# Performance work log

Measured on AMD Instinct MI355X. Metric: run time of the kernel, lower is better.

## Reference

```python
import jax, jax.numpy as jnp
import numpy as np

E = 1024
H = 16
D = E // H  # head_dim = 64
FF = 4 * E
EPS = 1e-5


def layernorm(x, g, b):
    mu = jnp.mean(x, axis=-1, keepdims=True)
    var = jnp.var(x, axis=-1, keepdims=True)
    return (x - mu) * jax.lax.rsqrt(var + EPS) * g + b


def setup_inputs() -> dict:
    key = jax.random.key(0)
    ks = jax.random.split(key, 12)
    s = 1.0 / np.sqrt(E)
    sf = 1.0 / np.sqrt(FF)
    return {
        "x": jax.random.normal(ks[0], (2, 2048, E), dtype=jnp.float32),
        "wq": jax.random.uniform(ks[1], (E, E), jnp.float32, -s, s),
        "wk": jax.random.uniform(ks[2], (E, E), jnp.float32, -s, s),
        "wv": jax.random.uniform(ks[3], (E, E), jnp.float32, -s, s),
        "wo": jax.random.uniform(ks[4], (E, E), jnp.float32, -s, s),
        "bo": jax.random.uniform(ks[5], (E,), jnp.float32, -s, s),
        "g1": jnp.ones((E,), jnp.float32),
        "b1": jnp.zeros((E,), jnp.float32),
        "w1": jax.random.uniform(ks[6], (FF, E), jnp.float32, -s, s),
        "bf1": jax.random.uniform(ks[7], (FF,), jnp.float32, -s, s),
        "w2": jax.random.uniform(ks[8], (E, FF), jnp.float32, -sf, sf),
        "bf2": jax.random.uniform(ks[9], (E,), jnp.float32, -sf, sf),
        "g2": jnp.ones((E,), jnp.float32),
        "b2": jnp.zeros((E,), jnp.float32),
    }


def reference(x, wq, wk, wv, wo, bo, g1, b1, w1, bf1, w2, bf2, g2, b2):
    B, L, _ = x.shape
    # projections (torch Linear: x @ W.T)
    q = (x @ wq.T).reshape(B, L, H, D).transpose(0, 2, 1, 3)  # (B,H,L,D)
    k = (x @ wk.T).reshape(B, L, H, D).transpose(0, 2, 1, 3)
    v = (x @ wv.T).reshape(B, L, H, D).transpose(0, 2, 1, 3)
    scores = jnp.einsum('bhqd,bhkd->bhqk', q, k) / np.sqrt(D)
    attn = jax.nn.softmax(scores, axis=-1)
    ctx = jnp.einsum('bhqk,bhkd->bhqd', attn, v)
    ctx = ctx.transpose(0, 2, 1, 3).reshape(B, L, E)
    attn_out = ctx @ wo.T + bo
    h = layernorm(x + attn_out, g1, b1)
    ff = jax.nn.gelu(h @ w1.T + bf1, approximate=False) @ w2.T + bf2
    return layernorm(h + ff, g2, b2)
```

## Files before the change

### kernel.cpp

```cpp
#include <hip/hip_runtime.h>
#include <hip/hip_bf16.h>
#include <stdint.h>

typedef __bf16 bf16x8 __attribute__((ext_vector_type(8)));
typedef float  f32x4  __attribute__((ext_vector_type(4)));
typedef unsigned short u16;
typedef u16 u16x8 __attribute__((ext_vector_type(8)));

__device__ __forceinline__ u16 f2b(float f) {
  uint32_t u = __builtin_bit_cast(uint32_t, f);
  u += 0x7fffu + ((u >> 16) & 1u);
  return (u16)(u >> 16);
}

__device__ __forceinline__ f32x4 mfma16(bf16x8 a, bf16x8 b, f32x4 c) {
  return __builtin_amdgcn_mfma_f32_16x16x32_bf16(a, b, c, 0, 0, 0);
}

__device__ __forceinline__ void gload_lds16(const void* g, void* l) {
  __builtin_amdgcn_global_load_lds(
      (const __attribute__((address_space(1))) void*)g,
      (__attribute__((address_space(3))) void*)l, 16, 0, 0);
}

#define BARRIER() asm volatile("s_barrier" ::: "memory")
#define LGKM0()   asm volatile("s_waitcnt lgkmcnt(0)" ::: "memory")

__global__ void f2b_all(const float* __restrict__ x,  const float* __restrict__ wq,
                        const float* __restrict__ wk, const float* __restrict__ wv,
                        const float* __restrict__ wo, const float* __restrict__ w1,
                        const float* __restrict__ w2,
                        u16* __restrict__ xb, u16* __restrict__ wqkvb,
                        u16* __restrict__ wob, u16* __restrict__ w1b,
                        u16* __restrict__ w2b) {
  const int i = blockIdx.x * blockDim.x + threadIdx.x;
  const float* src; u16* dst; int off;
  if (i < 524288)        { src = x;  dst = xb;              off = i; }
  else if (i < 655360)   { src = wq; dst = wqkvb;           off = i - 524288; }
  else if (i < 786432)   { src = wk; dst = wqkvb + 1048576; off = i - 655360; }
  else if (i < 917504)   { src = wv; dst = wqkvb + 2097152; off = i - 786432; }
  else if (i < 1048576)  { src = wo; dst = wob;             off = i - 917504; }
  else if (i < 1572864)  { src = w1; dst = w1b;             off = i - 1048576; }
  else                   { src = w2; dst = w2b;             off = i - 1572864; }
  const float4* p = (const float4*)src + (size_t)off * 2;
  float4 a = p[0], b = p[1];
  u16x8 r;
  r[0] = f2b(a.x); r[1] = f2b(a.y); r[2] = f2b(a.z); r[3] = f2b(a.w);
  r[4] = f2b(b.x); r[5] = f2b(b.y); r[6] = f2b(b.z); r[7] = f2b(b.w);
  *((u16x8*)dst + off) = r;
}

template<int MODE>
__global__ __launch_bounds__(512, 2) void gemm256(
    const u16* __restrict__ A, const u16* __restrict__ W,
    const float* __restrict__ bias,
    void* __restrict__ o0, void* __restrict__ o1,
    void* __restrict__ o2, void* __restrict__ o3,
    int Nsz, int Kstride, int Klen, int ntiles)
{
  __shared__ u16 As[2][2][8192];
  __shared__ u16 Bs[2][2][8192];

  const int nbn = Nsz >> 8;
  int bid = blockIdx.x;
  bid = (bid & 7) * ((int)gridDim.x >> 3) + (bid >> 3);
  const int tile = (MODE == 1) ? (bid % ntiles) : bid;
  const int sid  = (MODE == 1) ? (bid / ntiles) : 0;
  const int koff = sid * Klen;
  const int bm = tile / nbn;
  const int bn = tile % nbn;
  const int tid = threadIdx.x;
  const int w = tid >> 6, l = tid & 63;
  const int lh = l >> 4, ll = l & 15;
  const int wm = w >> 2, wn = w & 3;

  f32x4 acc[8][4] = {};

  const u16* Ag = A + (size_t)(bm * 256) * Kstride + koff;
  const u16* Wg = W + (size_t)(bn * 256) * Kstride + koff;

  const int r0 = tid >> 3, s0 = tid & 7;
  const int sg = s0 ^ (r0 & 7);
  const int NT = Klen >> 6;

  auto stage = [&](int t, int H) {
    const int b = t & 1;
    const size_t ce = (size_t)t * 64 + sg * 8;
    const u16* G = (H < 2) ? Ag : Wg;
    u16* D = (H < 2) ? &As[b][H & 1][0] : &Bs[b][H & 1][0];
    const int gr = (H & 1) * 128;
    gload_lds16(G + (size_t)(gr + r0) * Kstride + ce, D + tid * 8);
    gload_lds16(G + (size_t)(gr + r0 + 64) * Kstride + ce, D + (512 + tid) * 8);
  };

  auto dsA = [&](int p, int mi, int kk) -> bf16x8 {
    const int r = mi * 16 + ll;
    return *(const bf16x8*)(&As[p][wm][0] + r * 64 + (((kk * 4 + lh) ^ (ll & 7)) * 8));
  };
  auto dsB = [&](int p, int ni, int kk) -> bf16x8 {
    const int r = (wn & 1) * 64 + ni * 16 + ll;
    return *(const bf16x8*)(&Bs[p][wn >> 1][0] + r * 64 + (((kk * 4 + lh) ^ (ll & 7)) * 8));
  };

  stage(0, 0); stage(0, 1); stage(0, 2); stage(0, 3);
  asm volatile("s_waitcnt vmcnt(0)" ::: "memory");
  BARRIER();

  bf16x8 bq[4], aq[4];
  for (int t = 0; t < NT; ++t) {
    const int p = t & 1;
    const bool st = (t + 1 < NT);

#pragma unroll
    for (int ni = 0; ni < 4; ++ni) bq[ni] = dsB(p, ni, 0);
#pragma unroll
    for (int m2 = 0; m2 < 4; ++m2) aq[m2] = dsA(p, m2, 0);
    if (st) stage(t + 1, 0);
    BARRIER(); LGKM0();
    __builtin_amdgcn_s_setprio(1);
#pragma unroll
    for (int m2 = 0; m2 < 4; ++m2)
#pragma unroll
      for (int ni = 0; ni < 4; ++ni)
        acc[m2][ni] = mfma16(aq[m2], bq[ni], acc[m2][ni]);
    __builtin_amdgcn_s_setprio(0);
    BARRIER();

#pragma unroll
    for (int m2 = 0; m2 < 4; ++m2) aq[m2] = dsA(p, 4 + m2, 0);
    if (st) stage(t + 1, 1);
    BARRIER(); LGKM0();
    __builtin_amdgcn_s_setprio(1);
#pragma unroll
    for (int m2 = 0; m2 < 4; ++m2)
#pragma unroll
      for (int ni = 0; ni < 4; ++ni)
        acc[4 + m2][ni] = mfma16(aq[m2], bq[ni], acc[4 + m2][ni]);
    __builtin_amdgcn_s_setprio(0);
    BARRIER();

#pragma unroll
    for (int ni = 0; ni < 4; ++ni) bq[ni] = dsB(p, ni, 1);
#pragma unroll
    for (int m2 = 0; m2 < 4; ++m2) aq[m2] = dsA(p, m2, 1);
    if (st) stage(t + 1, 2);
    BARRIER(); LGKM0();
    __builtin_amdgcn_s_setprio(1);
#pragma unroll
    for (int m2 = 0; m2 < 4; ++m2)
#pragma unroll
      for (int ni = 0; ni < 4; ++ni)
        acc[m2][ni] = mfma16(aq[m2], bq[ni], acc[m2][ni]);
    __builtin_amdgcn_s_setprio(0);
    BARRIER();

#pragma unroll
    for (int m2 = 0; m2 < 4; ++m2) aq[m2] = dsA(p, 4 + m2, 1);
    if (st) stage(t + 1, 3);
    BARRIER(); LGKM0();
    __builtin_amdgcn_s_setprio(1);
#pragma unroll
    for (int m2 = 0; m2 < 4; ++m2)
#pragma unroll
      for (int ni = 0; ni < 4; ++ni)
        acc[4 + m2][ni] = mfma16(aq[m2], bq[ni], acc[4 + m2][ni]);
    __builtin_amdgcn_s_setprio(0);
    if (st) asm volatile("s_waitcnt vmcnt(0)" ::: "memory");
    BARRIER();
  }

#pragma unroll
  for (int mi = 0; mi < 8; ++mi) {
#pragma unroll
    for (int ni = 0; ni < 4; ++ni) {
      const int col = bn * 256 + wn * 64 + ni * 16 + ll;
#pragma unroll
      for (int i = 0; i < 4; ++i) {
        const int row = bm * 256 + wm * 128 + mi * 16 + lh * 4 + i;
        float v = acc[mi][ni][i];
        if (MODE == 1) {
          float* dst = (sid == 0) ? (float*)o0 : (sid == 1) ? (float*)o1
                     : (sid == 2) ? (float*)o2 : (float*)o3;
          dst[(size_t)row * Nsz + col] = v;
        } else if (MODE == 2) {
          float xx = v + bias[col];
          float gl = 0.5f * xx * (1.0f + erff(xx * 0.70710678118654752f));
          ((u16*)o0)[(size_t)row * Nsz + col] = f2b(gl);
        } else {
          const int which = col >> 10;
          const int e = col & 1023;
          const int hh = e >> 6, dd = e & 63;
          const int bb = row >> 11, nl = row & 2047;
          if (which == 0) {
            ((u16*)o0)[((size_t)(bb * 16 + hh) * 2048 + nl) * 64 + dd] = f2b(v * 0.18033688f);
          } else if (which == 1) {
            ((u16*)o1)[((size_t)(bb * 16 + hh) * 2048 + nl) * 64 + dd] = f2b(v);
          } else {
            ((u16*)o2)[((size_t)(bb * 16 + hh) * 64 + dd) * 2048 + nl] = f2b(v);
          }
        }
      }
    }
  }
}

__global__ __launch_bounds__(256, 4) void attn_fwd(
    const u16* __restrict__ Q, const u16* __restrict__ K,
    const u16* __restrict__ Vt, u16* __restrict__ ctx)
{
  __shared__ u16 Ks[2][64 * 64];
  __shared__ u16 Vs[2][64 * 64];
  __shared__ u16 Ps[4][16 * 64];

  const int bh = blockIdx.x & 31;
  const int qt = blockIdx.x >> 5;
  const int tid = threadIdx.x;
  const int w = tid >> 6, l = tid & 63;
  const int lh = l >> 4, ll = l & 15;
  const int q0 = qt * 64 + w * 16;

  bf16x8 qf[2];
  {
    const u16* Qg = Q + ((size_t)bh * 2048 + q0 + ll) * 64;
#pragma unroll
    for (int kk = 0; kk < 2; ++kk)
      qf[kk] = *(const bf16x8*)(Qg + kk * 32 + lh * 8);
  }

  bf16x8 ones;
  {
    const u16 o = 0x3F80;
#pragma unroll
    for (int i = 0; i < 8; ++i) ones[i] = __builtin_bit_cast(__bf16, o);
  }

  f32x4 cacc[4] = {};
  f32x4 lacc = {};
  float m_l = -1e30f;
  u16* ps = Ps[w];

  const int f0 = tid, f1 = 256 + tid;
  const int r0 = f0 >> 3, s0 = f0 & 7, g0 = (s0 ^ (r0 & 7)) * 8;
  const int r1 = f1 >> 3, s1 = f1 & 7, g1 = (s1 ^ (r1 & 7)) * 8;

  {
    gload_lds16(K + ((size_t)bh * 2048 + r0) * 64 + g0, Ks[0] + f0 * 8);
    gload_lds16(Vt + ((size_t)bh * 64 + r0) * 2048 + g0, Vs[0] + f0 * 8);
    gload_lds16(K + ((size_t)bh * 2048 + r1) * 64 + g1, Ks[0] + f1 * 8);
    gload_lds16(Vt + ((size_t)bh * 64 + r1) * 2048 + g1, Vs[0] + f1 * 8);
  }
  __syncthreads();

  for (int kt = 0; kt < 32; ++kt) {
    const int b = kt & 1;
    if (kt < 31) {
      const int kn = (kt + 1) * 64;
      gload_lds16(K + ((size_t)bh * 2048 + kn + r0) * 64 + g0, Ks[b ^ 1] + f0 * 8);
      gload_lds16(Vt + ((size_t)bh * 64 + r0) * 2048 + kn + g0, Vs[b ^ 1] + f0 * 8);
      gload_lds16(K + ((size_t)bh * 2048 + kn + r1) * 64 + g1, Ks[b ^ 1] + f1 * 8);
      gload_lds16(Vt + ((size_t)bh * 64 + r1) * 2048 + kn + g1, Vs[b ^ 1] + f1 * 8);
    }

    f32x4 st[4];
    __builtin_amdgcn_s_setprio(1);
#pragma unroll
    for (int jb = 0; jb < 4; ++jb) {
      f32x4 a = {};
#pragma unroll
      for (int kk = 0; kk < 2; ++kk) {
        const int r = jb * 16 + ll;
        bf16x8 kf = *(const bf16x8*)(Ks[b] + r * 64 + (((kk * 4 + lh) ^ (r & 7)) * 8));
        a = mfma16(kf, qf[kk], a);
      }
      st[jb] = a;
    }
    __builtin_amdgcn_s_setprio(0);

    float mx = fmaxf(fmaxf(fmaxf(st[0][0], st[0][1]), fmaxf(st[0][2], st[0][3])),
                     fmaxf(fmaxf(st[1][0], st[1][1]), fmaxf(st[1][2], st[1][3])));
    mx = fmaxf(mx, fmaxf(fmaxf(fmaxf(st[2][0], st[2][1]), fmaxf(st[2][2], st[2][3])),
                         fmaxf(fmaxf(st[3][0], st[3][1]), fmaxf(st[3][2], st[3][3]))));
    mx = fmaxf(mx, __shfl_xor(mx, 16));
    mx = fmaxf(mx, __shfl_xor(mx, 32));

    if (!__all(mx - m_l <= 8.0f)) {
      const float mn = fmaxf(m_l, mx);
      const float al = __builtin_amdgcn_exp2f(m_l - mn);
      m_l = mn;
      float alq[4];
#pragma unroll
      for (int i = 0; i < 4; ++i) alq[i] = __shfl(al, lh * 4 + i);
#pragma unroll
      for (int db = 0; db < 4; ++db)
#pragma unroll
        for (int i = 0; i < 4; ++i) cacc[db][i] *= alq[i];
#pragma unroll
      for (int i = 0; i < 4; ++i) lacc[i] *= alq[i];
    }

#pragma unroll
    for (int jb = 0; jb < 4; ++jb) {
      const float p0 = __builtin_amdgcn_exp2f(st[jb][0] - m_l);
      const float p1 = __builtin_amdgcn_exp2f(st[jb][1] - m_l);
      const float p2 = __builtin_amdgcn_exp2f(st[jb][2] - m_l);
      const float p3 = __builtin_amdgcn_exp2f(st[jb][3] - m_l);
      uint2 pk;
      asm("v_cvt_pk_bf16_f32 %0, %1, %2" : "=v"(pk.x) : "v"(p0), "v"(p1));
      asm("v_cvt_pk_bf16_f32 %0, %1, %2" : "=v"(pk.y) : "v"(p2), "v"(p3));
      *(uint2*)(ps + ll * 64 + (((jb * 2 + (lh >> 1)) ^ (ll & 7)) * 8) + (lh & 1) * 4) = pk;
    }

    asm volatile("s_waitcnt lgkmcnt(0)" ::: "memory");
    __builtin_amdgcn_sched_barrier(0);

    __builtin_amdgcn_s_setprio(1);
#pragma unroll
    for (int kk = 0; kk < 2; ++kk) {
      bf16x8 pf = *(const bf16x8*)(ps + ll * 64 + (((kk * 4 + lh) ^ (ll & 7)) * 8));
      lacc = mfma16(pf, ones, lacc);
#pragma unroll
      for (int db = 0; db < 4; ++db) {
        const int vr = db * 16 + ll;
        bf16x8 vf = *(const bf16x8*)(Vs[b] + vr * 64 + (((kk * 4 + lh) ^ (vr & 7)) * 8));
        cacc[db] = mfma16(pf, vf, cacc[db]);
      }
    }
    __builtin_amdgcn_s_setprio(0);
    __syncthreads();
  }

  const int bb = bh >> 4, hh = bh & 15;
#pragma unroll
  for (int db = 0; db < 4; ++db)
#pragma unroll
    for (int i = 0; i < 4; ++i) {
      const float v = cacc[db][i] / lacc[i];
      const size_t orow = (size_t)bb * 2048 + q0 + lh * 4 + i;
      const size_t ocol = (size_t)hh * 64 + db * 16 + ll;
      ctx[orow * 1024 + ocol] = f2b(v);
    }
}

__global__ __launch_bounds__(256) void ln_fused(
    const float* __restrict__ a,  const float* __restrict__ b0,
    const float* __restrict__ b1, const float* __restrict__ b2,
    const float* __restrict__ b3, const float* __restrict__ bias,
    const float* __restrict__ g,  const float* __restrict__ be,
    float* __restrict__ ho, u16* __restrict__ hb)
{
  const int row = blockIdx.x;
  const int t = threadIdx.x;
  const size_t base = (size_t)row * 1024 + t * 4;
  float4 xa = *(const float4*)(a + base);
  float4 xb = *(const float4*)(b0 + base);
  float v0 = xa.x + xb.x, v1 = xa.y + xb.y, v2 = xa.z + xb.z, v3 = xa.w + xb.w;
  if (b1) {
    float4 xc = *(const float4*)(b1 + base);
    v0 += xc.x; v1 += xc.y; v2 += xc.z; v3 += xc.w;
  }
  if (b2) {
    float4 xc = *(const float4*)(b2 + base);
    v0 += xc.x; v1 += xc.y; v2 += xc.z; v3 += xc.w;
  }
  if (b3) {
    float4 xc = *(const float4*)(b3 + base);
    v0 += xc.x; v1 += xc.y; v2 += xc.z; v3 += xc.w;
  }
  if (bias) {
    float4 xd = *(const float4*)(bias + t * 4);
    v0 += xd.x; v1 += xd.y; v2 += xd.z; v3 += xd.w;
  }
  float s = v0 + v1 + v2 + v3;
  float ss = v0 * v0 + v1 * v1 + v2 * v2 + v3 * v3;
#pragma unroll
  for (int d = 1; d < 64; d <<= 1) {
    s += __shfl_xor(s, d);
    ss += __shfl_xor(ss, d);
  }
  __shared__ float red[8];
  const int w = t >> 6, lid = t & 63;
  if (lid == 0) { red[w] = s; red[4 + w] = ss; }
  __syncthreads();
  s = red[0] + red[1] + red[2] + red[3];
  ss = red[4] + red[5] + red[6] + red[7];
  const float mean = s * (1.0f / 1024.0f);
  const float var = ss * (1.0f / 1024.0f) - mean * mean;
  const float rstd = rsqrtf(var + 1e-5f);
  const float vv[4] = {v0, v1, v2, v3};
#pragma unroll
  for (int i = 0; i < 4; ++i) {
    const int col = t * 4 + i;
    const float hv = (vv[i] - mean) * rstd * g[col] + be[col];
    if (ho) ho[base + i] = hv;
    if (hb) hb[base + i] = f2b(hv);
  }
}

extern "C" void kernel_launch(void* const* d_in, const int* in_sizes, int n_in,
                              void* d_out, int out_size, void* d_ws, size_t ws_size,
                              hipStream_t stream) {
  const float* x   = (const float*)d_in[0];
  const float* wq  = (const float*)d_in[1];
  const float* wk  = (const float*)d_in[2];
  const float* wv  = (const float*)d_in[3];
  const float* wo  = (const float*)d_in[4];
  const float* bo  = (const float*)d_in[5];
  const float* g1  = (const float*)d_in[6];
  const float* b1  = (const float*)d_in[7];
  const float* w1  = (const float*)d_in[8];
  const float* bf1 = (const float*)d_in[9];
  const float* w2  = (const float*)d_in[10];
  const float* bf2 = (const float*)d_in[11];
  const float* g2  = (const float*)d_in[12];
  const float* b2  = (const float*)d_in[13];

  char* ws = (char*)d_ws;
  const size_t MB = 1u << 20;
  u16* xb    = (u16*)(ws + 0);
  u16* wqkv  = (u16*)(ws + 8 * MB);
  u16* wob   = (u16*)(ws + 14 * MB);
  u16* w1b   = (u16*)(ws + 16 * MB);
  u16* w2b   = (u16*)(ws + 24 * MB);
  u16* qb    = (u16*)(ws + 32 * MB);
  u16* kb    = (u16*)(ws + 40 * MB);
  u16* vtb   = (u16*)(ws + 48 * MB);
  u16* ctxb  = (u16*)(ws + 56 * MB);
  float* pA   = (float*)(ws + 64 * MB);
  float* hbuf = (float*)(ws + 80 * MB);
  u16* hbb   = (u16*)(ws + 96 * MB);
  float* wo_p1 = (float*)(ws + 32 * MB);
  u16* ff1   = (u16*)(ws + 32 * MB);
  float* f2_p1 = (float*)(ws + 0);
  float* f2_p2 = (float*)(ws + 48 * MB);
  float* f2_p3 = (float*)d_out;

  f2b_all<<<8192, 256, 0, stream>>>(x, wq, wk, wv, wo, w1, w2, xb, wqkv, wob, w1b, w2b);

  gemm256<0><<<192, 512, 0, stream>>>(xb, wqkv, nullptr, qb, kb, vtb, nullptr,
                                      3072, 1024, 1024, 0);
  attn_fwd<<<1024, 256, 0, stream>>>(qb, kb, vtb, ctxb);
  gemm256<1><<<128, 512, 0, stream>>>(ctxb, wob, nullptr, pA, wo_p1, nullptr, nullptr,
                                      1024, 1024, 512, 64);
  ln_fused<<<4096, 256, 0, stream>>>(x, pA, wo_p1, nullptr, nullptr, bo, g1, b1, hbuf, hbb);
  gemm256<2><<<256, 512, 0, stream>>>(hbb, w1b, bf1, ff1, nullptr, nullptr, nullptr,
                                      4096, 1024, 1024, 0);
  gemm256<1><<<256, 512, 0, stream>>>(ff1, w2b, nullptr, pA, f2_p1, f2_p2, f2_p3,
                                      1024, 4096, 1024, 64);
  ln_fused<<<4096, 256, 0, stream>>>(hbuf, pA, f2_p1, f2_p2, f2_p3, bf2, g2, b2,
                                     (float*)d_out, nullptr);
}
```

Measured before the change: 294.0 us.

## Restage GEMM LDS by K-halves with partial vmcnt waits and 2-way FF2 split-K

```diff
diff --git a/kernel.cpp b/kernel.cpp
--- a/kernel.cpp
+++ b/kernel.cpp
@@ -58,8 +58,8 @@
     void* __restrict__ o2, void* __restrict__ o3,
     int Nsz, int Kstride, int Klen, int ntiles)
 {
-  __shared__ u16 As[2][2][8192];
-  __shared__ u16 Bs[2][2][8192];
+  __shared__ u16 As[2][2][256 * 32];
+  __shared__ u16 Bs[2][2][256 * 32];
 
   const int nbn = Nsz >> 8;
   int bid = blockIdx.x;
@@ -79,34 +79,33 @@
   const u16* Ag = A + (size_t)(bm * 256) * Kstride + koff;
   const u16* Wg = W + (size_t)(bn * 256) * Kstride + koff;
 
-  const int r0 = tid >> 3, s0 = tid & 7;
-  const int sg = s0 ^ (r0 & 7);
+  const int r0 = tid >> 2;
+  const int sg = (tid & 3) ^ (r0 & 3);
   const int NT = Klen >> 6;
 
   auto stage = [&](int t, int H) {
-    const int b = t & 1;
-    const size_t ce = (size_t)t * 64 + sg * 8;
-    const u16* G = (H < 2) ? Ag : Wg;
-    u16* D = (H < 2) ? &As[b][H & 1][0] : &Bs[b][H & 1][0];
-    const int gr = (H & 1) * 128;
-    gload_lds16(G + (size_t)(gr + r0) * Kstride + ce, D + tid * 8);
-    gload_lds16(G + (size_t)(gr + r0 + 64) * Kstride + ce, D + (512 + tid) * 8);
+    const int b = t & 1, kk = H >> 1;
+    const u16* G = (H & 1) ? Wg : Ag;
+    u16* D = (H & 1) ? &Bs[b][kk][0] : &As[b][kk][0];
+    const size_t ce = (size_t)t * 64 + kk * 32 + sg * 8;
+    gload_lds16(G + (size_t)r0 * Kstride + ce,         D + tid * 8);
+    gload_lds16(G + (size_t)(r0 + 128) * Kstride + ce, D + (512 + tid) * 8);
   };
 
   auto dsA = [&](int p, int mi, int kk) -> bf16x8 {
-    const int r = mi * 16 + ll;
-    return *(const bf16x8*)(&As[p][wm][0] + r * 64 + (((kk * 4 + lh) ^ (ll & 7)) * 8));
+    const int r = wm * 128 + mi * 16 + ll;
+    return *(const bf16x8*)(&As[p][kk][0] + r * 32 + ((lh ^ (ll & 3)) * 8));
   };
   auto dsB = [&](int p, int ni, int kk) -> bf16x8 {
-    const int r = (wn & 1) * 64 + ni * 16 + ll;
-    return *(const bf16x8*)(&Bs[p][wn >> 1][0] + r * 64 + (((kk * 4 + lh) ^ (ll & 7)) * 8));
+    const int r = wn * 64 + ni * 16 + ll;
+    return *(const bf16x8*)(&Bs[p][kk][0] + r * 32 + ((lh ^ (ll & 3)) * 8));
   };
 
   stage(0, 0); stage(0, 1); stage(0, 2); stage(0, 3);
   asm volatile("s_waitcnt vmcnt(0)" ::: "memory");
   BARRIER();
 
-  bf16x8 bq[4], aq[4];
+  bf16x8 aq[4], bq[4];
   for (int t = 0; t < NT; ++t) {
     const int p = t & 1;
     const bool st = (t + 1 < NT);
@@ -116,7 +115,7 @@
 #pragma unroll
     for (int m2 = 0; m2 < 4; ++m2) aq[m2] = dsA(p, m2, 0);
     if (st) stage(t + 1, 0);
-    BARRIER(); LGKM0();
+    BARRIER(); LGKM0(); __builtin_amdgcn_sched_barrier(0);
     __builtin_amdgcn_s_setprio(1);
 #pragma unroll
     for (int m2 = 0; m2 < 4; ++m2)
@@ -129,7 +128,7 @@
 #pragma unroll
     for (int m2 = 0; m2 < 4; ++m2) aq[m2] = dsA(p, 4 + m2, 0);
     if (st) stage(t + 1, 1);
-    BARRIER(); LGKM0();
+    BARRIER(); LGKM0(); __builtin_amdgcn_sched_barrier(0);
     __builtin_amdgcn_s_setprio(1);
 #pragma unroll
     for (int m2 = 0; m2 < 4; ++m2)
@@ -137,6 +136,8 @@
       for (int ni = 0; ni < 4; ++ni)
         acc[4 + m2][ni] = mfma16(aq[m2], bq[ni], acc[4 + m2][ni]);
     __builtin_amdgcn_s_setprio(0);
+    if (st) asm volatile("s_waitcnt vmcnt(4)" ::: "memory");
+    else    asm volatile("s_waitcnt vmcnt(0)" ::: "memory");
     BARRIER();
 
 #pragma unroll
@@ -144,7 +145,7 @@
 #pragma unroll
     for (int m2 = 0; m2 < 4; ++m2) aq[m2] = dsA(p, m2, 1);
     if (st) stage(t + 1, 2);
-    BARRIER(); LGKM0();
+    BARRIER(); LGKM0(); __builtin_amdgcn_sched_barrier(0);
     __builtin_amdgcn_s_setprio(1);
 #pragma unroll
     for (int m2 = 0; m2 < 4; ++m2)
@@ -157,7 +158,7 @@
 #pragma unroll
     for (int m2 = 0; m2 < 4; ++m2) aq[m2] = dsA(p, 4 + m2, 1);
     if (st) stage(t + 1, 3);
-    BARRIER(); LGKM0();
+    BARRIER(); LGKM0(); __builtin_amdgcn_sched_barrier(0);
     __builtin_amdgcn_s_setprio(1);
 #pragma unroll
     for (int m2 = 0; m2 < 4; ++m2)
@@ -165,7 +166,8 @@
       for (int ni = 0; ni < 4; ++ni)
         acc[4 + m2][ni] = mfma16(aq[m2], bq[ni], acc[4 + m2][ni]);
     __builtin_amdgcn_s_setprio(0);
-    if (st) asm volatile("s_waitcnt vmcnt(0)" ::: "memory");
+    if (st) asm volatile("s_waitcnt vmcnt(4)" ::: "memory");
+    else    asm volatile("s_waitcnt vmcnt(0)" ::: "memory");
     BARRIER();
   }
 
@@ -431,8 +433,6 @@
   float* wo_p1 = (float*)(ws + 32 * MB);
   u16* ff1   = (u16*)(ws + 32 * MB);
   float* f2_p1 = (float*)(ws + 0);
-  float* f2_p2 = (float*)(ws + 48 * MB);
-  float* f2_p3 = (float*)d_out;
 
   f2b_all<<<8192, 256, 0, stream>>>(x, wq, wk, wv, wo, w1, w2, xb, wqkv, wob, w1b, w2b);
 
@@ -444,8 +444,8 @@
   ln_fused<<<4096, 256, 0, stream>>>(x, pA, wo_p1, nullptr, nullptr, bo, g1, b1, hbuf, hbb);
   gemm256<2><<<256, 512, 0, stream>>>(hbb, w1b, bf1, ff1, nullptr, nullptr, nullptr,
                                       4096, 1024, 1024, 0);
-  gemm256<1><<<256, 512, 0, stream>>>(ff1, w2b, nullptr, pA, f2_p1, f2_p2, f2_p3,
-                                      1024, 4096, 1024, 64);
-  ln_fused<<<4096, 256, 0, stream>>>(hbuf, pA, f2_p1, f2_p2, f2_p3, bf2, g2, b2,
+  gemm256<1><<<128, 512, 0, stream>>>(ff1, w2b, nullptr, pA, f2_p1, nullptr, nullptr,
+                                      1024, 4096, 2048, 64);
+  ln_fused<<<4096, 256, 0, stream>>>(hbuf, pA, f2_p1, nullptr, nullptr, bf2, g2, b2,
                                      (float*)d_out, nullptr);
 }
```

Measured after the change: 317.9 us. 8.1% more time.
